# Performance work log

Measured on AMD Instinct MI355X. Metric: run time of the kernel, lower is better.

Reference implementation:

```python
import jax, jax.numpy as jnp
import numpy as np
import math

NUM_HEADS = 16
HEAD_DIM = 64

def setup_inputs() -> dict:
    key = jax.random.key(0)
    k1, = jax.random.split(key, 1)
    x = jax.random.normal(k1, (4, 4096, NUM_HEADS, HEAD_DIM), dtype=jnp.float32)
    log_amp = jnp.zeros((NUM_HEADS,), dtype=jnp.float32)
    log_decay = jnp.full((NUM_HEADS,), math.log(0.3), dtype=jnp.float32)
    mix_logit = jnp.zeros((NUM_HEADS,), dtype=jnp.float32)
    return {"x": x, "log_amp": log_amp, "log_decay": log_decay, "mix_logit": mix_logit}

def _next_power_of_two(v: int) -> int:
    return 1 << (v - 1).bit_length()

def reference(x, log_amp, log_decay, mix_logit):
    B, L, H, D = x.shape
    n_fft = _next_power_of_two(2 * L)  # 8192 for L=4096
    # b l h d -> b h d l
    xf = jnp.transpose(x, (0, 2, 3, 1)).astype(jnp.float32)
    F = jnp.fft.rfft(xf, n=n_fft, axis=-1)  # [B,H,D,n_fft//2+1] complex64
    freq = jnp.arange(F.shape[-1], dtype=jnp.float32)
    amp = jax.nn.softplus(log_amp)[None, :, None, None]
    decay = jax.nn.softplus(log_decay)[None, :, None, None] + 1e-4
    # minimum-phase power-law filter: |H| = amp/(1+w^2)^(decay/2), phase = -decay*atan(w)
    mag = amp / jnp.power(1.0 + freq * freq, decay * 0.5)
    phase = -decay * jnp.arctan(freq)
    filt = (mag * jnp.cos(phase) + 1j * (mag * jnp.sin(phase))).astype(F.dtype)
    y = jnp.fft.irfft(F * filt, n=n_fft, axis=-1)[..., :L]
    y = jnp.transpose(y, (0, 3, 1, 2)).astype(x.dtype)  # b h d l -> b l h d
    mix = jax.nn.sigmoid(mix_logit)[None, None, :, None]
    return mix * y + (1.0 - mix) * x
```

## Files before the change

### kernel.cpp

```cpp
#include <hip/hip_runtime.h>
#include <math.h>

namespace {
constexpr int kB = 4;
constexpr int kL = 4096;
constexpr int kH = 16;
constexpr int kD = 64;
constexpr int kC = kH * kD;
constexpr int kM = 4096;
constexpr int NTH = 256;
constexpr int kTabIters = 9;

__device__ __forceinline__ float2 cmul(float2 a, float2 b) {
  return make_float2(a.x * b.x - a.y * b.y, a.x * b.y + a.y * b.x);
}
__device__ __forceinline__ float2 cadd(float2 a, float2 b) { return make_float2(a.x + b.x, a.y + b.y); }
__device__ __forceinline__ float2 csub(float2 a, float2 b) { return make_float2(a.x - b.x, a.y - b.y); }
__device__ __forceinline__ float2 cconj(float2 a) { return make_float2(a.x, -a.y); }
__device__ __forceinline__ float2 cmuli(float2 a) { return make_float2(-a.y, a.x); }
__device__ __forceinline__ float2 cscale(float2 a, float s) { return make_float2(a.x * s, a.y * s); }

typedef float cplx __attribute__((ext_vector_type(2)));

__device__ __forceinline__ cplx pk_add(cplx a, cplx b) {
  cplx r;
  asm("v_pk_add_f32 %0, %1, %2" : "=v"(r) : "v"(a), "v"(b));
  return r;
}
__device__ __forceinline__ cplx pk_sub(cplx a, cplx b) {
  cplx r;
  asm("v_pk_add_f32 %0, %1, %2 neg_lo:[0,1] neg_hi:[0,1]" : "=v"(r) : "v"(a), "v"(b));
  return r;
}
__device__ __forceinline__ cplx pk_addpi(cplx a, cplx b) {
  cplx r;
  asm("v_pk_add_f32 %0, %1, %2 op_sel:[0,1] op_sel_hi:[1,0] neg_lo:[0,1]" : "=v"(r) : "v"(a), "v"(b));
  return r;
}
__device__ __forceinline__ cplx pk_addmi(cplx a, cplx b) {
  cplx r;
  asm("v_pk_add_f32 %0, %1, %2 op_sel:[0,1] op_sel_hi:[1,0] neg_hi:[0,1]" : "=v"(r) : "v"(a), "v"(b));
  return r;
}
__device__ __forceinline__ cplx pk_cmul(cplx a, cplx b) {
  cplx t, r;
  asm("v_pk_mul_f32 %0, %1, %2 op_sel:[0,0] op_sel_hi:[0,1]" : "=v"(t) : "v"(a), "v"(b));
  asm("v_pk_fma_f32 %0, %1, %2, %3 op_sel:[1,1,0] op_sel_hi:[1,0,1] neg_lo:[0,1,0]"
      : "=v"(r) : "v"(a), "v"(b), "v"(t));
  return r;
}

__device__ __forceinline__ unsigned dr4(unsigned p) {
  unsigned r = __brev(p) >> 20;
  return ((r & 0x555u) << 1) | ((r >> 1) & 0x555u);
}
__device__ __forceinline__ unsigned dr16(unsigned p) {
  return ((p & 15u) << 8) | (p & 0xF0u) | (p >> 8);
}
__device__ __forceinline__ int SW(int i) { return i ^ ((i >> 4) & 15); }
#define POS(k) ((((k) & 3) << 2) | ((k) >> 2))

__device__ __forceinline__ int IDX(int i) { return i + (i >> 4); }
constexpr int kZPad = kM + (kM >> 4);

#define TW_TREE(w)                                                            \
  cplx W1 = (w), W2 = pk_cmul(W1, W1), W4 = pk_cmul(W2, W2),                  \
       W8 = pk_cmul(W4, W4);                                                  \
  cplx W3 = pk_cmul(W2, W1), W5 = pk_cmul(W4, W1), W6 = pk_cmul(W4, W2),      \
       W7 = pk_cmul(W4, W3);                                                  \
  cplx W9 = pk_cmul(W8, W1), W10 = pk_cmul(W8, W2), W11 = pk_cmul(W8, W3),    \
       W12 = pk_cmul(W8, W4);                                                 \
  cplx W13 = pk_cmul(W8, W5), W14 = pk_cmul(W8, W6), W15 = pk_cmul(W8, W7);

#define TW_APPLY(r)                                                           \
  r[POS(1)] = pk_cmul(r[POS(1)], W1);   r[POS(2)] = pk_cmul(r[POS(2)], W2);   \
  r[POS(3)] = pk_cmul(r[POS(3)], W3);   r[POS(4)] = pk_cmul(r[POS(4)], W4);   \
  r[POS(5)] = pk_cmul(r[POS(5)], W5);   r[POS(6)] = pk_cmul(r[POS(6)], W6);   \
  r[POS(7)] = pk_cmul(r[POS(7)], W7);   r[POS(8)] = pk_cmul(r[POS(8)], W8);   \
  r[POS(9)] = pk_cmul(r[POS(9)], W9);   r[POS(10)] = pk_cmul(r[POS(10)], W10);\
  r[POS(11)] = pk_cmul(r[POS(11)], W11); r[POS(12)] = pk_cmul(r[POS(12)], W12);\
  r[POS(13)] = pk_cmul(r[POS(13)], W13); r[POS(14)] = pk_cmul(r[POS(14)], W14);\
  r[POS(15)] = pk_cmul(r[POS(15)], W15);

#define TWS_TREE(b0, w)                                                       \
  cplx P2 = pk_cmul(w, w), P4 = pk_cmul(P2, P2), P8 = pk_cmul(P4, P4);        \
  cplx B0 = (b0), B1 = pk_cmul(b0, w), B2 = pk_cmul(B0, P2),                  \
       B3 = pk_cmul(B1, P2);                                                  \
  cplx B4 = pk_cmul(B0, P4), B5 = pk_cmul(B1, P4), B6 = pk_cmul(B2, P4),      \
       B7 = pk_cmul(B3, P4);                                                  \
  cplx B8 = pk_cmul(B0, P8), B9 = pk_cmul(B1, P8), B10 = pk_cmul(B2, P8),     \
       B11 = pk_cmul(B3, P8);                                                 \
  cplx B12 = pk_cmul(B4, P8), B13 = pk_cmul(B5, P8), B14 = pk_cmul(B6, P8),   \
       B15 = pk_cmul(B7, P8);

#define TWS_APPLY(r)                                                          \
  r[POS(0)] = pk_cmul(r[POS(0)], B0);   r[POS(1)] = pk_cmul(r[POS(1)], B1);   \
  r[POS(2)] = pk_cmul(r[POS(2)], B2);   r[POS(3)] = pk_cmul(r[POS(3)], B3);   \
  r[POS(4)] = pk_cmul(r[POS(4)], B4);   r[POS(5)] = pk_cmul(r[POS(5)], B5);   \
  r[POS(6)] = pk_cmul(r[POS(6)], B6);   r[POS(7)] = pk_cmul(r[POS(7)], B7);   \
  r[POS(8)] = pk_cmul(r[POS(8)], B8);   r[POS(9)] = pk_cmul(r[POS(9)], B9);   \
  r[POS(10)] = pk_cmul(r[POS(10)], B10); r[POS(11)] = pk_cmul(r[POS(11)], B11);\
  r[POS(12)] = pk_cmul(r[POS(12)], B12); r[POS(13)] = pk_cmul(r[POS(13)], B13);\
  r[POS(14)] = pk_cmul(r[POS(14)], B14); r[POS(15)] = pk_cmul(r[POS(15)], B15);

__device__ __forceinline__ float2 filt_val(float k, float ampS, float dec) {
  float mag = ampS * __expf(-0.5f * dec * log1pf(k * k));
  float ph = -dec * atanf(k);
  float s, c;
  __sincosf(ph, &s, &c);
  return make_float2(mag * c, mag * s);
}

template <int S, bool HZ>
__device__ __forceinline__ void fft16(cplx r[16]) {
  constexpr float C1 = 0.92387953251128674f;
  constexpr float S1 = 0.38268343236508978f;
  constexpr float R2 = 0.70710678118654752f;
  const float sg = (float)S;
  const cplx Wa = {C1, sg * S1};
  const cplx Wb = {R2, sg * R2};
  const cplx Wc = {S1, sg * C1};
  const cplx Wd = {-R2, sg * R2};
  const cplx We = {-C1, -sg * S1};
#pragma unroll
  for (int n2 = 0; n2 < 4; ++n2) {
    cplx t0, t1, t2, t3;
    if (HZ) {
      t0 = r[n2]; t1 = r[n2]; t2 = r[n2 + 4]; t3 = r[n2 + 4];
    } else {
      cplx a0 = r[n2], a1 = r[n2 + 4], a2 = r[n2 + 8], a3 = r[n2 + 12];
      t0 = pk_add(a0, a2); t1 = pk_sub(a0, a2); t2 = pk_add(a1, a3); t3 = pk_sub(a1, a3);
    }
    cplx u0 = pk_add(t0, t2);
    cplx u2 = pk_sub(t0, t2);
    cplx u1 = (S < 0) ? pk_addmi(t1, t3) : pk_addpi(t1, t3);
    cplx u3 = (S < 0) ? pk_addpi(t1, t3) : pk_addmi(t1, t3);
    if (n2 == 0) { r[0] = u0; r[4] = u1; r[8] = u2; r[12] = u3; }
    if (n2 == 1) { r[1] = u0; r[5] = pk_cmul(u1, Wa); r[9] = pk_cmul(u2, Wb); r[13] = pk_cmul(u3, Wc); }
    if (n2 == 2) {
      r[2] = u0; r[6] = pk_cmul(u1, Wb);
      cplx m;
      if (S < 0) { m.x = u2.y; m.y = -u2.x; } else { m.x = -u2.y; m.y = u2.x; }
      r[10] = m;
      r[14] = pk_cmul(u3, Wd);
    }
    if (n2 == 3) { r[3] = u0; r[7] = pk_cmul(u1, Wc); r[11] = pk_cmul(u2, Wd); r[15] = pk_cmul(u3, We); }
  }
#pragma unroll
  for (int s = 0; s < 4; ++s) {
    cplx b0 = r[4 * s], b1 = r[4 * s + 1], b2 = r[4 * s + 2], b3 = r[4 * s + 3];
    cplx t0 = pk_add(b0, b2), t1 = pk_sub(b0, b2), t2 = pk_add(b1, b3), t3 = pk_sub(b1, b3);
    r[4 * s] = pk_add(t0, t2);
    r[4 * s + 2] = pk_sub(t0, t2);
    r[4 * s + 1] = (S < 0) ? pk_addmi(t1, t3) : pk_addpi(t1, t3);
    r[4 * s + 3] = (S < 0) ? pk_addpi(t1, t3) : pk_addmi(t1, t3);
  }
}

__device__ __forceinline__ void pw_pair(float2 Zk, float2 Zmk, int k, float ampS, float dec,
                                        float2* Wk, float2* Wmk) {
  float2 A = cscale(cadd(Zk, cconj(Zmk)), 0.5f);
  float2 Bv = cscale(csub(Zk, cconj(Zmk)), 0.5f);
  float sn, cs;
  __sincosf(-3.14159265358979323846f * (float)k / (float)kM, &sn, &cs);
  float2 tw = make_float2(cs, sn);
  float2 P = cmuli(cmul(tw, Bv));
  float2 Xk = csub(A, P);
  float2 Xmk = cconj(cadd(A, P));
  float2 Yk = cmul(Xk, filt_val((float)k, ampS, dec));
  float2 Ymk = cmul(Xmk, filt_val((float)(kM - k), ampS, dec));
  float2 Ev = cscale(cadd(Yk, cconj(Ymk)), 0.5f);
  float2 Ov = cscale(cmul(cconj(tw), csub(Yk, cconj(Ymk))), 0.5f);
  float2 iO = cmuli(Ov);
  *Wk = cadd(Ev, iO);
  *Wmk = cconj(csub(Ev, iO));
}
}

__global__ __launch_bounds__(256) void build_table(const float* __restrict__ la,
                                                   const float* __restrict__ ld,
                                                   float2* __restrict__ tab) {
  const int i = blockIdx.x;
  const int h = blockIdx.y;
  const int t = threadIdx.x;
  float av = la[h], dv = ld[h];
  float amp = (av > 20.f) ? av : log1pf(__expf(av));
  float dec = ((dv > 20.f) ? dv : log1pf(__expf(dv))) + 1e-4f;
  float ampS = amp * (1.0f / (float)kM);
  float2 e0 = make_float2(0.f, 0.f), e1 = e0, e2 = e0, e3 = e0;
  const int c = t & 15;
  if (i == 0 && t == 0) {
    float F0 = filt_val(0.f, ampS, dec).x;
    float FM = filt_val((float)kM, ampS, dec).x;
    e0 = make_float2(0.5f * (F0 + FM), 0.5f * (F0 - FM));
    e1 = make_float2(0.5f * (F0 - FM), 0.5f * (F0 + FM));
  } else if (i == 0 && t == 8) {
    e0 = cconj(filt_val((float)(kM / 2), ampS, dec));
  } else if ((i >= 1 && i <= 7) || c < 8) {
    int p = (i << 8) + t;
    int k = (int)dr16((unsigned)p);
    float2 a, b, g, d;
    pw_pair(make_float2(1.f, 0.f), make_float2(0.f, 0.f), k, ampS, dec, &a, &g);
    pw_pair(make_float2(0.f, 0.f), make_float2(1.f, 0.f), k, ampS, dec, &b, &d);
    e0 = a; e1 = b; e2 = g; e3 = d;
  }
  float2* e = tab + ((size_t)(h * kTabIters + i) * 256 + t) * 4;
  e[0] = e0; e[1] = e1; e[2] = e2; e[3] = e3;
}

__global__ __launch_bounds__(256) void transpose_fwd(const float* __restrict__ in,
                                                     float* __restrict__ outp) {
  __shared__ float T[32][33];
  const int b = blockIdx.z;
  const int r0 = blockIdx.x * 32;
  const int c0 = blockIdx.y * 32;
  const float* ib = in + (size_t)b * kL * kC;
  float* ob = outp + (size_t)b * kC * kL;
  const int tx = threadIdx.x & 31, ty = threadIdx.x >> 5;
  for (int i = 0; i < 32; i += 8)
    T[ty + i][tx] = ib[(size_t)(r0 + ty + i) * kC + c0 + tx];
  __syncthreads();
  for (int i = 0; i < 32; i += 8)
    ob[(size_t)(c0 + ty + i) * kL + r0 + tx] = T[tx][ty + i];
}

__global__ __launch_bounds__(NTH) void fft_rows(float* __restrict__ ws,
                                                const float2* __restrict__ tab) {
  __shared__ cplx Z[kM];
  const int row = blockIdx.x;
  const int h = (row >> 6) & (kH - 1);
  const int t = threadIdx.x;
  cplx* xrow = (cplx*)(ws + (size_t)row * kL);

  cplx r[16];
  const int swt = t ^ ((t >> 4) & 15);

#pragma unroll
  for (int j = 0; j < 8; ++j) r[j] = xrow[t + 256 * j];
  fft16<-1, true>(r);
  {
    float sn, cs;
    __sincosf(-6.283185307179586f * (float)t / 4096.f, &sn, &cs);
    cplx w = {cs, sn};
    TW_TREE(w);
    TW_APPLY(r);
    cplx* Zb = &Z[swt];
#pragma unroll
    for (int k1 = 0; k1 < 16; ++k1) Zb[k1 << 8] = r[POS(k1)];
  }
  __syncthreads();

  {
    const int g = t >> 4, m2 = t & 15;
    const int base = g << 8;
#pragma unroll
    for (int m1 = 0; m1 < 16; ++m1) r[m1] = Z[base + (m1 << 4) + (m2 ^ m1)];
    fft16<-1, false>(r);
    float sn, cs;
    __sincosf(-6.283185307179586f * (float)m2 / 256.f, &sn, &cs);
    cplx w = {cs, sn};
    TW_TREE(w);
    TW_APPLY(r);
#pragma unroll
    for (int j1 = 0; j1 < 16; ++j1) Z[base + (j1 << 4) + (m2 ^ j1)] = r[POS(j1)];
  }
  __syncthreads();

  {
    const int g = t >> 4, j1 = t & 15;
    const int base = (g << 8) + (j1 << 4);
#pragma unroll
    for (int m2 = 0; m2 < 16; ++m2) r[m2] = Z[base + (m2 ^ j1)];
    fft16<-1, false>(r);
#pragma unroll
    for (int j2 = 0; j2 < 16; ++j2) Z[base + (j2 ^ j1)] = r[POS(j2)];
  }
  __syncthreads();

  {
    const int c = t & 15;
    const float4* tpz = (const float4*)(tab + (size_t)h * kTabIters * 256 * 4);
#pragma unroll
    for (int i = 0; i <= 8; ++i) {
      const float4* tp = tpz + ((i << 8) + t) * 2;
      float4 q0 = tp[0], q1 = tp[1];
      if (i == 0 && t == 0) {
        cplx Z0 = Z[0];
        cplx o; o.x = q0.x * Z0.x + q0.y * Z0.y; o.y = q0.z * Z0.x + q0.w * Z0.y;
        Z[0] = o;
      } else if (i == 0 && t == 8) {
        cplx f; f.x = q0.x; f.y = q0.y;
        Z[8] = pk_cmul(f, Z[8]);
      } else if ((i >= 1 && i <= 7) || c < 8) {
        int p = (i << 8) + t;
        int p2 = (i == 0) ? ((t < 16) ? (16 - t) : (271 - t))
                          : (((16 - i) << 8) + (255 - t));
        int sp = SW(p), sp2 = SW(p2);
        cplx Zk = Z[sp], Zmk = Z[sp2];
        cplx e0 = {q0.x, q0.y}, e1 = {q0.z, q0.w};
        cplx e2 = {q1.x, q1.y}, e3 = {q1.z, q1.w};
        cplx cZk = {Zk.x, -Zk.y}, cZmk = {Zmk.x, -Zmk.y};
        Z[sp] = pk_add(pk_cmul(e0, Zk), pk_cmul(e1, cZmk));
        Z[sp2] = pk_add(pk_cmul(e2, cZk), pk_cmul(e3, Zmk));
      }
    }
  }
  __syncthreads();

  {
    const int k1 = t >> 4, j1 = t & 15;
    const int base = (k1 << 8) + (j1 << 4);
#pragma unroll
    for (int j2 = 0; j2 < 16; ++j2) r[j2] = Z[base + (j2 ^ j1)];
    fft16<1, false>(r);
    float sn, cs;
    __sincosf(6.283185307179586f * (float)j1 / 256.f, &sn, &cs);
    cplx w = {cs, sn};
    TW_TREE(w);
    TW_APPLY(r);
#pragma unroll
    for (int m2 = 0; m2 < 16; ++m2) Z[base + (m2 ^ j1)] = r[POS(m2)];
  }
  __syncthreads();

  {
    const int k1 = t >> 4, m2 = t & 15;
#pragma unroll
    for (int j1 = 0; j1 < 16; ++j1) r[j1] = Z[(k1 << 8) + (j1 << 4) + (m2 ^ j1)];
    fft16<1, false>(r);
    float sn, cs;
    __sincosf(6.283185307179586f * (float)(k1 * m2) / 4096.f, &sn, &cs);
    cplx b0 = {cs, sn};
    __sincosf(6.283185307179586f * (float)k1 / 256.f, &sn, &cs);
    cplx w = {cs, sn};
    TWS_TREE(b0, w);
    TWS_APPLY(r);
#pragma unroll
    for (int m1 = 0; m1 < 16; ++m1) Z[(k1 << 8) + (m1 << 4) + (m2 ^ m1)] = r[POS(m1)];
  }
  __syncthreads();

  {
    cplx* Zb = &Z[swt];
#pragma unroll
    for (int k1 = 0; k1 < 16; ++k1) r[k1] = Zb[k1 << 8];
    fft16<1, false>(r);
#pragma unroll
    for (int n1 = 0; n1 < 8; ++n1) xrow[(n1 << 8) + t] = r[POS(n1)];
  }
}

__global__ __launch_bounds__(256) void mix_out(const float* __restrict__ yT,
                                               const float* __restrict__ x,
                                               const float* __restrict__ mix_logit,
                                               float* __restrict__ outp) {
  __shared__ float T[32][33];
  const int b = blockIdx.z;
  const int r0 = blockIdx.x * 32;
  const int c0 = blockIdx.y * 32;
  const int h = c0 >> 6;
  const float ml = mix_logit[h];
  const float mix = 1.0f / (1.0f + __expf(-ml));
  const float omix = 1.0f - mix;
  const float* yb = yT + (size_t)b * kC * kL;
  const float* xb = x + (size_t)b * kL * kC;
  float* ob = outp + (size_t)b * kL * kC;
  const int tx = threadIdx.x & 31, ty = threadIdx.x >> 5;
  for (int i = 0; i < 32; i += 8)
    T[ty + i][tx] = yb[(size_t)(c0 + ty + i) * kL + r0 + tx];
  __syncthreads();
  for (int i = 0; i < 32; i += 8) {
    size_t idx = (size_t)(r0 + ty + i) * kC + c0 + tx;
    ob[idx] = mix * T[tx][ty + i] + omix * xb[idx];
  }
}

__global__ __launch_bounds__(NTH) void fftconv_fallback(
    const float* __restrict__ x, const float* __restrict__ log_amp,
    const float* __restrict__ log_decay, const float* __restrict__ mix_logit,
    float* __restrict__ out) {
  __shared__ float2 Z[kZPad];
  const int row = blockIdx.x;
  const int d = row & (kD - 1);
  const int h = (row >> 6) & (kH - 1);
  const int b = row >> 10;
  const int t = threadIdx.x;
  const size_t rowoff = (size_t)b * kL * kC + (size_t)h * kD + (size_t)d;
  const float* xrow = x + rowoff;
  float* orow = out + rowoff;

  const float av = log_amp[h];
  const float dv = log_decay[h];
  const float amp = (av > 20.f) ? av : log1pf(__expf(av));
  const float dec = ((dv > 20.f) ? dv : log1pf(__expf(dv))) + 1e-4f;
  const float ampS = amp * (1.0f / (float)kM);
  const float ml = mix_logit[h];
  const float mix = 1.0f / (1.0f + __expf(-ml));
  const float omix = 1.0f - mix;

  for (int i = 0; i < kM / NTH; ++i) {
    int n = t + i * NTH;
    float2 z;
    if (n < kL / 2) {
      z.x = xrow[(size_t)(2 * n) * kC];
      z.y = xrow[(size_t)(2 * n + 1) * kC];
    } else {
      z = make_float2(0.f, 0.f);
    }
    Z[IDX(n)] = z;
  }
  __syncthreads();

  for (int Ls = kM; Ls >= 4; Ls >>= 2) {
    const int q = Ls >> 2;
    const float wstep = -6.283185307179586f / (float)Ls;
    for (int i = 0; i < kM / 4 / NTH; ++i) {
      int bt = t + i * NTH;
      int jj = bt & (q - 1);
      int base = ((bt - jj) << 2) + jj;
      float2 a = Z[IDX(base)], bb = Z[IDX(base + q)];
      float2 c = Z[IDX(base + 2 * q)], dd = Z[IDX(base + 3 * q)];
      float2 t0 = cadd(a, c), t1 = csub(a, c), t2 = cadd(bb, dd), t3 = csub(bb, dd);
      float2 u0 = cadd(t0, t2), u2 = csub(t0, t2);
      float2 it3 = cmuli(t3);
      float2 u1 = csub(t1, it3), u3 = cadd(t1, it3);
      float sn, cs;
      __sincosf(wstep * (float)jj, &sn, &cs);
      float2 w1 = make_float2(cs, sn);
      float2 w2 = cmul(w1, w1);
      float2 w3 = cmul(w2, w1);
      Z[IDX(base)] = u0;
      Z[IDX(base + q)] = cmul(u1, w1);
      Z[IDX(base + 2 * q)] = cmul(u2, w2);
      Z[IDX(base + 3 * q)] = cmul(u3, w3);
    }
    __syncthreads();
  }

  for (int i = 0; i <= kM / 2 / NTH; ++i) {
    int k = t + i * NTH;
    if (k > kM / 2) continue;
    if (k == 0) {
      float2 Z0 = Z[IDX(0)];
      float X0 = Z0.x + Z0.y;
      float XM = Z0.x - Z0.y;
      float2 f0 = filt_val(0.f, ampS, dec);
      float2 fM = filt_val((float)kM, ampS, dec);
      float Y0 = X0 * f0.x;
      float YM = XM * fM.x;
      Z[IDX(0)] = make_float2(0.5f * (Y0 + YM), 0.5f * (Y0 - YM));
    } else if (k == kM / 2) {
      unsigned p = dr4(kM / 2);
      float2 Zk = Z[IDX(p)];
      float2 f = filt_val((float)(kM / 2), ampS, dec);
      float2 Y = cmul(cconj(Zk), f);
      Z[IDX(p)] = cconj(Y);
    } else {
      unsigned pk = dr4((unsigned)k), pmk = dr4((unsigned)(kM - k));
      float2 Zk = Z[IDX(pk)], Zmk = Z[IDX(pmk)];
      float2 A = cscale(cadd(Zk, cconj(Zmk)), 0.5f);
      float2 Bv = cscale(csub(Zk, cconj(Zmk)), 0.5f);
      float sn, cs;
      __sincosf(-3.14159265358979323846f * (float)k / (float)kM, &sn, &cs);
      float2 tw = make_float2(cs, sn);
      float2 P = cmuli(cmul(tw, Bv));
      float2 Xk = csub(A, P);
      float2 Xmk = cconj(cadd(A, P));
      float2 Yk = cmul(Xk, filt_val((float)k, ampS, dec));
      float2 Ymk = cmul(Xmk, filt_val((float)(kM - k), ampS, dec));
      float2 Ev = cscale(cadd(Yk, cconj(Ymk)), 0.5f);
      float2 Ov = cscale(cmul(cconj(tw), csub(Yk, cconj(Ymk))), 0.5f);
      float2 iO = cmuli(Ov);
      Z[IDX(pk)] = cadd(Ev, iO);
      Z[IDX(pmk)] = cconj(csub(Ev, iO));
    }
  }
  __syncthreads();

  for (int Ls = 4; Ls <= kM; Ls <<= 2) {
    const int q = Ls >> 2;
    const float wstep = 6.283185307179586f / (float)Ls;
    for (int i = 0; i < kM / 4 / NTH; ++i) {
      int bt = t + i * NTH;
      int jj = bt & (q - 1);
      int base = ((bt - jj) << 2) + jj;
      float sn, cs;
      __sincosf(wstep * (float)jj, &sn, &cs);
      float2 w1 = make_float2(cs, sn);
      float2 w2 = cmul(w1, w1);
      float2 w3 = cmul(w2, w1);
      float2 a = Z[IDX(base)];
      float2 bb = cmul(Z[IDX(base + q)], w1);
      float2 c = cmul(Z[IDX(base + 2 * q)], w2);
      float2 dd = cmul(Z[IDX(base + 3 * q)], w3);
      float2 s0 = cadd(a, c), s1 = csub(a, c), s2 = cadd(bb, dd), s3 = csub(bb, dd);
      float2 is3 = cmuli(s3);
      Z[IDX(base)] = cadd(s0, s2);
      Z[IDX(base + 2 * q)] = csub(s0, s2);
      Z[IDX(base + q)] = cadd(s1, is3);
      Z[IDX(base + 3 * q)] = csub(s1, is3);
    }
    __syncthreads();
  }

  for (int i = 0; i < kL / 2 / NTH; ++i) {
    int n = t + i * NTH;
    float2 w = Z[IDX(n)];
    size_t i0 = (size_t)(2 * n) * kC;
    float x0 = xrow[i0];
    float x1 = xrow[i0 + kC];
    orow[i0] = mix * w.x + omix * x0;
    orow[i0 + kC] = mix * w.y + omix * x1;
  }
}

extern "C" void kernel_launch(void* const* d_in, const int* in_sizes, int n_in,
                              void* d_out, int out_size, void* d_ws, size_t ws_size,
                              hipStream_t stream) {
  const float* x = (const float*)d_in[0];
  const float* la = (const float*)d_in[1];
  const float* ld = (const float*)d_in[2];
  const float* ml = (const float*)d_in[3];
  float* out = (float*)d_out;
  const size_t ybytes = (size_t)kB * kC * kL * sizeof(float);
  const size_t tabbytes = (size_t)kH * kTabIters * 256 * 4 * sizeof(float2);
  if (ws_size >= ybytes + tabbytes) {
    float* ws = (float*)d_ws;
    float2* tab = (float2*)((char*)d_ws + ybytes);
    build_table<<<dim3(kTabIters, kH), dim3(256), 0, stream>>>(la, ld, tab);
    transpose_fwd<<<dim3(kL / 32, kC / 32, kB), dim3(256), 0, stream>>>(x, ws);
    fft_rows<<<dim3(kB * kC), dim3(NTH), 0, stream>>>(ws, tab);
    mix_out<<<dim3(kL / 32, kC / 32, kB), dim3(256), 0, stream>>>(ws, x, ml, out);
  } else {
    fftconv_fallback<<<dim3(kB * kC), dim3(NTH), 0, stream>>>(x, la, ld, ml, out);
  }
}
```

Baseline: 116.4 us.

## Store transposed intermediates as bf16 and precompute FFT twiddle tables

The transposed workspace between transpose, FFT and mix kernels now holds bf16 pairs instead of fp32, which halves the global traffic of the intermediate round trips. Per-thread twiddle trees built from sincos are replaced by loads from a precomputed twiddle table filled by a new small kernel. Rounding the input and output of the FFT to bf16 lowers precision and may exceed the tolerance. The table lookups add global loads in exchange for fewer complex multiplies.

After: 108.6 us. 1.07x faster.

```diff
diff --git a/kernel.cpp b/kernel.cpp
--- a/kernel.cpp
+++ b/kernel.cpp
@@ -8,6 +8,7 @@
 constexpr int kD = 64;
 constexpr int kC = kH * kD;
 constexpr int kM = 4096;
+constexpr int kN2 = kL / 2;
 constexpr int NTH = 256;
 constexpr int kTabIters = 9;
 
@@ -50,6 +51,18 @@
   return r;
 }
 
+__device__ __forceinline__ unsigned pkbf(float lo, float hi) {
+  unsigned r;
+  asm("v_cvt_pk_bf16_f32 %0, %1, %2" : "=v"(r) : "v"(lo), "v"(hi));
+  return r;
+}
+__device__ __forceinline__ cplx unpk(unsigned d) {
+  cplx r;
+  r.x = __uint_as_float(d << 16);
+  r.y = __uint_as_float(d & 0xffff0000u);
+  return r;
+}
+
 __device__ __forceinline__ unsigned dr4(unsigned p) {
   unsigned r = __brev(p) >> 20;
   return ((r & 0x555u) << 1) | ((r >> 1) & 0x555u);
@@ -62,46 +75,6 @@
 
 __device__ __forceinline__ int IDX(int i) { return i + (i >> 4); }
 constexpr int kZPad = kM + (kM >> 4);
-
-#define TW_TREE(w)                                                            \
-  cplx W1 = (w), W2 = pk_cmul(W1, W1), W4 = pk_cmul(W2, W2),                  \
-       W8 = pk_cmul(W4, W4);                                                  \
-  cplx W3 = pk_cmul(W2, W1), W5 = pk_cmul(W4, W1), W6 = pk_cmul(W4, W2),      \
-       W7 = pk_cmul(W4, W3);                                                  \
-  cplx W9 = pk_cmul(W8, W1), W10 = pk_cmul(W8, W2), W11 = pk_cmul(W8, W3),    \
-       W12 = pk_cmul(W8, W4);                                                 \
-  cplx W13 = pk_cmul(W8, W5), W14 = pk_cmul(W8, W6), W15 = pk_cmul(W8, W7);
-
-#define TW_APPLY(r)                                                           \
-  r[POS(1)] = pk_cmul(r[POS(1)], W1);   r[POS(2)] = pk_cmul(r[POS(2)], W2);   \
-  r[POS(3)] = pk_cmul(r[POS(3)], W3);   r[POS(4)] = pk_cmul(r[POS(4)], W4);   \
-  r[POS(5)] = pk_cmul(r[POS(5)], W5);   r[POS(6)] = pk_cmul(r[POS(6)], W6);   \
-  r[POS(7)] = pk_cmul(r[POS(7)], W7);   r[POS(8)] = pk_cmul(r[POS(8)], W8);   \
-  r[POS(9)] = pk_cmul(r[POS(9)], W9);   r[POS(10)] = pk_cmul(r[POS(10)], W10);\
-  r[POS(11)] = pk_cmul(r[POS(11)], W11); r[POS(12)] = pk_cmul(r[POS(12)], W12);\
-  r[POS(13)] = pk_cmul(r[POS(13)], W13); r[POS(14)] = pk_cmul(r[POS(14)], W14);\
-  r[POS(15)] = pk_cmul(r[POS(15)], W15);
-
-#define TWS_TREE(b0, w)                                                       \
-  cplx P2 = pk_cmul(w, w), P4 = pk_cmul(P2, P2), P8 = pk_cmul(P4, P4);        \
-  cplx B0 = (b0), B1 = pk_cmul(b0, w), B2 = pk_cmul(B0, P2),                  \
-       B3 = pk_cmul(B1, P2);                                                  \
-  cplx B4 = pk_cmul(B0, P4), B5 = pk_cmul(B1, P4), B6 = pk_cmul(B2, P4),      \
-       B7 = pk_cmul(B3, P4);                                                  \
-  cplx B8 = pk_cmul(B0, P8), B9 = pk_cmul(B1, P8), B10 = pk_cmul(B2, P8),     \
-       B11 = pk_cmul(B3, P8);                                                 \
-  cplx B12 = pk_cmul(B4, P8), B13 = pk_cmul(B5, P8), B14 = pk_cmul(B6, P8),   \
-       B15 = pk_cmul(B7, P8);
-
-#define TWS_APPLY(r)                                                          \
-  r[POS(0)] = pk_cmul(r[POS(0)], B0);   r[POS(1)] = pk_cmul(r[POS(1)], B1);   \
-  r[POS(2)] = pk_cmul(r[POS(2)], B2);   r[POS(3)] = pk_cmul(r[POS(3)], B3);   \
-  r[POS(4)] = pk_cmul(r[POS(4)], B4);   r[POS(5)] = pk_cmul(r[POS(5)], B5);   \
-  r[POS(6)] = pk_cmul(r[POS(6)], B6);   r[POS(7)] = pk_cmul(r[POS(7)], B7);   \
-  r[POS(8)] = pk_cmul(r[POS(8)], B8);   r[POS(9)] = pk_cmul(r[POS(9)], B9);   \
-  r[POS(10)] = pk_cmul(r[POS(10)], B10); r[POS(11)] = pk_cmul(r[POS(11)], B11);\
-  r[POS(12)] = pk_cmul(r[POS(12)], B12); r[POS(13)] = pk_cmul(r[POS(13)], B13);\
-  r[POS(14)] = pk_cmul(r[POS(14)], B14); r[POS(15)] = pk_cmul(r[POS(15)], B15);
 
 __device__ __forceinline__ float2 filt_val(float k, float ampS, float dec) {
   float mag = ampS * __expf(-0.5f * dec * log1pf(k * k));
@@ -208,42 +181,74 @@
   e[0] = e0; e[1] = e1; e[2] = e2; e[3] = e3;
 }
 
+__global__ __launch_bounds__(256) void build_tw(float2* __restrict__ tw) {
+  const int j = blockIdx.x;
+  const int t = threadIdx.x;
+  const float TP = 6.28318530717958647692f;
+  float s, c;
+  if (j < 15) {
+    sincosf(-TP * (float)((j + 1) * t) * (1.f / 4096.f), &s, &c);
+    tw[j * 256 + t] = make_float2(c, s);
+  }
+  {
+    int k1 = t >> 4, m2 = t & 15;
+    sincosf(TP * (float)(k1 * (m2 + 16 * j)) * (1.f / 4096.f), &s, &c);
+    tw[15 * 256 + j * 256 + t] = make_float2(c, s);
+  }
+  if (j < 15 && t < 16) {
+    sincosf(-TP * (float)((j + 1) * t) * (1.f / 256.f), &s, &c);
+    tw[31 * 256 + j * 16 + t] = make_float2(c, s);
+    tw[31 * 256 + 240 + j * 16 + t] = make_float2(c, -s);
+  }
+}
+
 __global__ __launch_bounds__(256) void transpose_fwd(const float* __restrict__ in,
-                                                     float* __restrict__ outp) {
-  __shared__ float T[32][33];
+                                                     unsigned* __restrict__ zout) {
+  __shared__ float T[64][33];
   const int b = blockIdx.z;
-  const int r0 = blockIdx.x * 32;
+  const int l0 = blockIdx.x * 64;
   const int c0 = blockIdx.y * 32;
   const float* ib = in + (size_t)b * kL * kC;
-  float* ob = outp + (size_t)b * kC * kL;
+  unsigned* ob = zout + (size_t)b * kC * kN2;
   const int tx = threadIdx.x & 31, ty = threadIdx.x >> 5;
-  for (int i = 0; i < 32; i += 8)
-    T[ty + i][tx] = ib[(size_t)(r0 + ty + i) * kC + c0 + tx];
-  __syncthreads();
-  for (int i = 0; i < 32; i += 8)
-    ob[(size_t)(c0 + ty + i) * kL + r0 + tx] = T[tx][ty + i];
-}
-
-__global__ __launch_bounds__(NTH) void fft_rows(float* __restrict__ ws,
-                                                const float2* __restrict__ tab) {
+#pragma unroll
+  for (int i = 0; i < 64; i += 8)
+    T[ty + i][tx] = ib[(size_t)(l0 + ty + i) * kC + c0 + tx];
+  __syncthreads();
+  const int n0 = l0 >> 1;
+#pragma unroll
+  for (int i = 0; i < 32; i += 8) {
+    int c = ty + i;
+    ob[(size_t)(c0 + c) * kN2 + n0 + tx] = pkbf(T[2 * tx][c], T[2 * tx + 1][c]);
+  }
+}
+
+__global__ __launch_bounds__(NTH) void fft_rows(unsigned* __restrict__ zio,
+                                                const float2* __restrict__ tab,
+                                                const cplx* __restrict__ twF1,
+                                                const cplx* __restrict__ twI2,
+                                                const cplx* __restrict__ twF2s,
+                                                const cplx* __restrict__ twI1s) {
   __shared__ cplx Z[kM];
   const int row = blockIdx.x;
   const int h = (row >> 6) & (kH - 1);
   const int t = threadIdx.x;
-  cplx* xrow = (cplx*)(ws + (size_t)row * kL);
-
-  cplx r[16];
+  unsigned* zrow = zio + (size_t)row * kN2;
+
+  cplx r[16], tw[15];
   const int swt = t ^ ((t >> 4) & 15);
 
-#pragma unroll
-  for (int j = 0; j < 8; ++j) r[j] = xrow[t + 256 * j];
-  fft16<-1, true>(r);
-  {
-    float sn, cs;
-    __sincosf(-6.283185307179586f * (float)t / 4096.f, &sn, &cs);
-    cplx w = {cs, sn};
-    TW_TREE(w);
-    TW_APPLY(r);
+  {
+    unsigned din[8];
+#pragma unroll
+    for (int j = 0; j < 8; ++j) din[j] = zrow[t + (j << 8)];
+#pragma unroll
+    for (int p = 1; p < 16; ++p) tw[p - 1] = twF1[((p - 1) << 8) + t];
+#pragma unroll
+    for (int j = 0; j < 8; ++j) r[j] = unpk(din[j]);
+    fft16<-1, true>(r);
+#pragma unroll
+    for (int p = 1; p < 16; ++p) r[POS(p)] = pk_cmul(r[POS(p)], tw[p - 1]);
     cplx* Zb = &Z[swt];
 #pragma unroll
     for (int k1 = 0; k1 < 16; ++k1) Zb[k1 << 8] = r[POS(k1)];
@@ -254,13 +259,12 @@
     const int g = t >> 4, m2 = t & 15;
     const int base = g << 8;
 #pragma unroll
+    for (int p = 1; p < 16; ++p) tw[p - 1] = twF2s[((p - 1) << 4) + m2];
+#pragma unroll
     for (int m1 = 0; m1 < 16; ++m1) r[m1] = Z[base + (m1 << 4) + (m2 ^ m1)];
     fft16<-1, false>(r);
-    float sn, cs;
-    __sincosf(-6.283185307179586f * (float)m2 / 256.f, &sn, &cs);
-    cplx w = {cs, sn};
-    TW_TREE(w);
-    TW_APPLY(r);
+#pragma unroll
+    for (int p = 1; p < 16; ++p) r[POS(p)] = pk_cmul(r[POS(p)], tw[p - 1]);
 #pragma unroll
     for (int j1 = 0; j1 < 16; ++j1) Z[base + (j1 << 4) + (m2 ^ j1)] = r[POS(j1)];
   }
@@ -311,13 +315,12 @@
     const int k1 = t >> 4, j1 = t & 15;
     const int base = (k1 << 8) + (j1 << 4);
 #pragma unroll
+    for (int p = 1; p < 16; ++p) tw[p - 1] = twI1s[((p - 1) << 4) + j1];
+#pragma unroll
     for (int j2 = 0; j2 < 16; ++j2) r[j2] = Z[base + (j2 ^ j1)];
     fft16<1, false>(r);
-    float sn, cs;
-    __sincosf(6.283185307179586f * (float)j1 / 256.f, &sn, &cs);
-    cplx w = {cs, sn};
-    TW_TREE(w);
-    TW_APPLY(r);
+#pragma unroll
+    for (int p = 1; p < 16; ++p) r[POS(p)] = pk_cmul(r[POS(p)], tw[p - 1]);
 #pragma unroll
     for (int m2 = 0; m2 < 16; ++m2) Z[base + (m2 ^ j1)] = r[POS(m2)];
   }
@@ -325,16 +328,14 @@
 
   {
     const int k1 = t >> 4, m2 = t & 15;
+    cplx twb[16];
+#pragma unroll
+    for (int m1 = 0; m1 < 16; ++m1) twb[m1] = twI2[(m1 << 8) + t];
 #pragma unroll
     for (int j1 = 0; j1 < 16; ++j1) r[j1] = Z[(k1 << 8) + (j1 << 4) + (m2 ^ j1)];
     fft16<1, false>(r);
-    float sn, cs;
-    __sincosf(6.283185307179586f * (float)(k1 * m2) / 4096.f, &sn, &cs);
-    cplx b0 = {cs, sn};
-    __sincosf(6.283185307179586f * (float)k1 / 256.f, &sn, &cs);
-    cplx w = {cs, sn};
-    TWS_TREE(b0, w);
-    TWS_APPLY(r);
+#pragma unroll
+    for (int m1 = 0; m1 < 16; ++m1) r[POS(m1)] = pk_cmul(r[POS(m1)], twb[m1]);
 #pragma unroll
     for (int m1 = 0; m1 < 16; ++m1) Z[(k1 << 8) + (m1 << 4) + (m2 ^ m1)] = r[POS(m1)];
   }
@@ -346,32 +347,43 @@
     for (int k1 = 0; k1 < 16; ++k1) r[k1] = Zb[k1 << 8];
     fft16<1, false>(r);
 #pragma unroll
-    for (int n1 = 0; n1 < 8; ++n1) xrow[(n1 << 8) + t] = r[POS(n1)];
-  }
-}
-
-__global__ __launch_bounds__(256) void mix_out(const float* __restrict__ yT,
+    for (int n1 = 0; n1 < 8; ++n1) {
+      cplx v = r[POS(n1)];
+      zrow[(n1 << 8) + t] = pkbf(v.x, v.y);
+    }
+  }
+}
+
+__global__ __launch_bounds__(256) void mix_out(const unsigned* __restrict__ zin,
                                                const float* __restrict__ x,
                                                const float* __restrict__ mix_logit,
                                                float* __restrict__ outp) {
-  __shared__ float T[32][33];
+  __shared__ float T[64][33];
   const int b = blockIdx.z;
-  const int r0 = blockIdx.x * 32;
+  const int l0 = blockIdx.x * 64;
   const int c0 = blockIdx.y * 32;
   const int h = c0 >> 6;
   const float ml = mix_logit[h];
   const float mix = 1.0f / (1.0f + __expf(-ml));
   const float omix = 1.0f - mix;
-  const float* yb = yT + (size_t)b * kC * kL;
+  const unsigned* yb = zin + (size_t)b * kC * kN2;
   const float* xb = x + (size_t)b * kL * kC;
   float* ob = outp + (size_t)b * kL * kC;
   const int tx = threadIdx.x & 31, ty = threadIdx.x >> 5;
-  for (int i = 0; i < 32; i += 8)
-    T[ty + i][tx] = yb[(size_t)(c0 + ty + i) * kL + r0 + tx];
-  __syncthreads();
+  const int n0 = l0 >> 1;
+#pragma unroll
   for (int i = 0; i < 32; i += 8) {
-    size_t idx = (size_t)(r0 + ty + i) * kC + c0 + tx;
-    ob[idx] = mix * T[tx][ty + i] + omix * xb[idx];
+    int c = ty + i;
+    unsigned d = yb[(size_t)(c0 + c) * kN2 + n0 + tx];
+    T[2 * tx][c] = __uint_as_float(d << 16);
+    T[2 * tx + 1][c] = __uint_as_float(d & 0xffff0000u);
+  }
+  __syncthreads();
+#pragma unroll
+  for (int i = 0; i < 64; i += 8) {
+    int l = ty + i;
+    size_t idx = (size_t)(l0 + l) * kC + c0 + tx;
+    ob[idx] = mix * T[l][tx] + omix * xb[idx];
   }
 }
 
@@ -522,15 +534,22 @@
   const float* ld = (const float*)d_in[2];
   const float* ml = (const float*)d_in[3];
   float* out = (float*)d_out;
-  const size_t ybytes = (size_t)kB * kC * kL * sizeof(float);
+  const size_t zbytes = (size_t)kB * kC * kN2 * sizeof(unsigned);
   const size_t tabbytes = (size_t)kH * kTabIters * 256 * 4 * sizeof(float2);
-  if (ws_size >= ybytes + tabbytes) {
-    float* ws = (float*)d_ws;
-    float2* tab = (float2*)((char*)d_ws + ybytes);
+  const size_t twbytes = (size_t)(31 * 256 + 480) * sizeof(float2);
+  if (ws_size >= zbytes + tabbytes + twbytes) {
+    unsigned* wsz = (unsigned*)d_ws;
+    float2* tab = (float2*)((char*)d_ws + zbytes);
+    float2* tw = (float2*)((char*)d_ws + zbytes + tabbytes);
+    const cplx* twF1 = (const cplx*)tw;
+    const cplx* twI2 = (const cplx*)(tw + 15 * 256);
+    const cplx* twF2s = (const cplx*)(tw + 31 * 256);
+    const cplx* twI1s = (const cplx*)(tw + 31 * 256 + 240);
     build_table<<<dim3(kTabIters, kH), dim3(256), 0, stream>>>(la, ld, tab);
-    transpose_fwd<<<dim3(kL / 32, kC / 32, kB), dim3(256), 0, stream>>>(x, ws);
-    fft_rows<<<dim3(kB * kC), dim3(NTH), 0, stream>>>(ws, tab);
-    mix_out<<<dim3(kL / 32, kC / 32, kB), dim3(256), 0, stream>>>(ws, x, ml, out);
+    build_tw<<<dim3(16), dim3(256), 0, stream>>>(tw);
+    transpose_fwd<<<dim3(kL / 64, kC / 32, kB), dim3(256), 0, stream>>>(x, wsz);
+    fft_rows<<<dim3(kB * kC), dim3(NTH), 0, stream>>>(wsz, tab, twF1, twI2, twF2s, twI1s);
+    mix_out<<<dim3(kL / 64, kC / 32, kB), dim3(256), 0, stream>>>(wsz, x, ml, out);
   } else {
     fftconv_fallback<<<dim3(kB * kC), dim3(NTH), 0, stream>>>(x, la, ld, ml, out);
   }
```
